# Optimization experiments

Measured on AMD Instinct MI355X. Metric: run time of the kernel, lower is better.

The kernel has to match this reference:

```python
import jax, jax.numpy as jnp
import numpy as np

D_MODEL = 1024
NHEAD = 16
EPS = 1e-5


def pos_embed(x, pos):
    # Faithful, vectorized form of the sparse rotation matrix in the source.
    # Source builds rot[..., i, i+1] = sin(pos*i*omega) for even i and
    # rot[..., i, i-1] = cos(pos*i*omega) for odd i, then contracts the feature
    # dim of x against the rotation (intended einsum 'btf,btfd->btd').
    # Resulting column j: even j <- x[..., j+1]*cos(pos*(j+1)*omega),
    #                     odd  j <- x[..., j-1]*sin(pos*(j-1)*omega).
    d = x.shape[-1]
    omega = jnp.pi / d
    i_even = jnp.arange(0, d, 2, dtype=x.dtype)   # even rows -> odd output cols (sin)
    i_odd = jnp.arange(1, d, 2, dtype=x.dtype)    # odd rows  -> even output cols (cos)
    p = pos[..., None]  # (L,B,1)
    sin_part = jnp.sin(p * i_even * omega) * x[..., 0::2]  # -> odd columns
    cos_part = jnp.cos(p * i_odd * omega) * x[..., 1::2]   # -> even columns
    # interleave: even col = cos_part, odd col = sin_part
    return jnp.stack([cos_part, sin_part], axis=-1).reshape(x.shape)


def layer_norm_eps(x, w, b):
    # Source uses torch.var default (unbiased, ddof=1)
    mean = jnp.mean(x, axis=-1, keepdims=True)
    var = jnp.var(x, axis=-1, keepdims=True, ddof=1)
    return w * (x - mean) / jnp.sqrt(var + EPS) + b


def mha(q, k, v, w_qkv, b_qkv, w_o, b_o, nhead):
    L, B, E = q.shape
    S = k.shape[0]
    hd = E // nhead
    wq, wk, wv = jnp.split(w_qkv, 3, axis=0)
    bq, bk, bv = jnp.split(b_qkv, 3, axis=0)
    qp = (q @ wq.T + bq).reshape(L, B, nhead, hd).transpose(1, 2, 0, 3)  # (B,h,L,hd)
    kp = (k @ wk.T + bk).reshape(S, B, nhead, hd).transpose(1, 2, 0, 3)
    vp = (v @ wv.T + bv).reshape(S, B, nhead, hd).transpose(1, 2, 0, 3)
    scale = jnp.asarray(1.0 / np.sqrt(hd), q.dtype)
    scores = jnp.einsum('bhld,bhsd->bhls', qp, kp) * scale
    attn = jax.nn.softmax(scores, axis=-1)
    out = jnp.einsum('bhls,bhsd->bhld', attn, vp)
    out = out.transpose(2, 0, 1, 3).reshape(L, B, E) @ w_o.T + b_o
    ws = attn.mean(axis=1)  # average over heads, torch default
    return out, ws


def setup_inputs() -> dict:
    key = jax.random.key(0)
    ks = jax.random.split(key, 16)
    T, S, B, E, FF = 1024, 1024, 4, D_MODEL, 4096
    sd = 0.02
    return {
        'tgt': jax.random.normal(ks[0], (T, B, E), jnp.float32),
        'memory': jax.random.normal(ks[1], (S, B, E), jnp.float32),
        'pos': jax.random.uniform(ks[2], (S, B), jnp.float32) * S,
        'query_pos': jax.random.uniform(ks[3], (T, B), jnp.float32) * T,
        'w_qkv_self': jax.random.normal(ks[4], (3 * E, E), jnp.float32) * sd,
        'b_qkv_self': jnp.zeros((3 * E,), jnp.float32),
        'w_o_self': jax.random.normal(ks[5], (E, E), jnp.float32) * sd,
        'b_o_self': jnp.zeros((E,), jnp.float32),
        'w_qkv_cross': jax.random.normal(ks[6], (3 * E, E), jnp.float32) * sd,
        'b_qkv_cross': jnp.zeros((3 * E,), jnp.float32),
        'w_o_cross': jax.random.normal(ks[7], (E, E), jnp.float32) * sd,
        'b_o_cross': jnp.zeros((E,), jnp.float32),
        'w1': jax.random.normal(ks[8], (FF, E), jnp.float32) * sd,
        'b1': jnp.zeros((FF,), jnp.float32),
        'w2': jax.random.normal(ks[9], (E, FF), jnp.float32) * sd,
        'b2': jnp.zeros((E,), jnp.float32),
        'g1': jnp.ones((E,), jnp.float32),
        'beta1': jnp.zeros((E,), jnp.float32),
        'g2': jnp.ones((E,), jnp.float32),
        'beta2': jnp.zeros((E,), jnp.float32),
    }


def reference(tgt, memory, pos, query_pos,
              w_qkv_self, b_qkv_self, w_o_self, b_o_self,
              w_qkv_cross, b_qkv_cross, w_o_cross, b_o_cross,
              w1, b1, w2, b2, g1, beta1, g2, beta2):
    # normalize_before=False, residual=True, dropout inactive (eval)
    qk = pos_embed(tgt, query_pos)
    tgt2, _ = mha(qk, qk, tgt, w_qkv_self, b_qkv_self, w_o_self, b_o_self, NHEAD)
    tgt = tgt + tgt2
    tgt = layer_norm_eps(tgt, g1, beta1)
    tgt2, ws = mha(pos_embed(tgt, query_pos), pos_embed(memory, pos), memory,
                   w_qkv_cross, b_qkv_cross, w_o_cross, b_o_cross, NHEAD)
    tgt = tgt + tgt2
    tgt = layer_norm_eps(tgt, g2, beta2)
    tgt2 = jax.nn.relu(tgt @ w1.T + b1) @ w2.T + b2
    tgt = tgt + tgt2
    return tgt, ws
```

## Files before the change

### kernel.cpp

```cpp
#include <hip/hip_runtime.h>

typedef unsigned short u16;
typedef __attribute__((ext_vector_type(8))) short short8;
typedef __attribute__((ext_vector_type(8))) unsigned short u16x8;
typedef __attribute__((ext_vector_type(4))) float f32x4;

#define GLOAD16(SRC, DST) __builtin_amdgcn_global_load_lds( \
    (const __attribute__((address_space(1))) void*)(SRC),   \
    (__attribute__((address_space(3))) void*)(DST), 16, 0, 0)

#define SWZ(BKv, r) ((BKv) == 32 ? (((r) >> 1) & 3) : ((r) & 7))

#define QSCALE 0.18033688011112042f

__device__ __forceinline__ u16 f2bf(float f) {
  union { float f; unsigned u; } v; v.f = f;
  unsigned r = v.u + 0x7fffu + ((v.u >> 16) & 1u);
  return (u16)(r >> 16);
}
__device__ __forceinline__ float bf2f(u16 h) {
  union { unsigned u; float f; } v; v.u = ((unsigned)h) << 16;
  return v.f;
}

__global__ __launch_bounds__(256) void wcvt_kernel(const float* __restrict__ s0,
                                                   const float* __restrict__ s1,
                                                   const float* __restrict__ s2,
                                                   const float* __restrict__ s3,
                                                   const float* __restrict__ s4,
                                                   const float* __restrict__ s5,
                                                   u16* __restrict__ dst) {
  long i = ((long)blockIdx.x * 256 + threadIdx.x) * 4;
  const float* src; long off;
  if (i < 3145728)        { src = s0; off = 0; }
  else if (i < 4194304)   { src = s1; off = 3145728; }
  else if (i < 7340032)   { src = s2; off = 4194304; }
  else if (i < 8388608)   { src = s3; off = 7340032; }
  else if (i < 12582912)  { src = s4; off = 8388608; }
  else                    { src = s5; off = 12582912; }
  float4 v = *(const float4*)(src + (i - off));
  ushort4 o; o.x = f2bf(v.x); o.y = f2bf(v.y); o.z = f2bf(v.z); o.w = f2bf(v.w);
  *(ushort4*)(dst + i) = o;
}

__global__ __launch_bounds__(256) void pos_embed_kernel(const float* __restrict__ x,
                                                        const float* __restrict__ pos,
                                                        u16* __restrict__ out,
                                                        u16* __restrict__ out2,
                                                        u16* __restrict__ raw) {
  int m = blockIdx.x;
  int tid = threadIdx.x;
  float p = pos[m];
  long base = ((long)m << 10);
  int j = tid * 4;
  float4 xv = *(const float4*)(x + base + j);
  const float inv = 1.0f / 2048.0f;
  float r0 = p * (float)(j + 0) * inv;
  float r1 = p * (float)(j + 1) * inv;
  float r2 = p * (float)(j + 2) * inv;
  float r3 = p * (float)(j + 3) * inv;
  float s1 = __builtin_amdgcn_sinf(r0 - floorf(r0));
  float c0 = __builtin_amdgcn_cosf(r1 - floorf(r1));
  float s3 = __builtin_amdgcn_sinf(r2 - floorf(r2));
  float c2 = __builtin_amdgcn_cosf(r3 - floorf(r3));
  ushort4 o;
  o.x = f2bf(c0 * xv.y);
  o.y = f2bf(s1 * xv.x);
  o.z = f2bf(c2 * xv.w);
  o.w = f2bf(s3 * xv.z);
  *(ushort4*)(out + base + j) = o;
  if (out2) *(ushort4*)(out2 + base + j) = o;
  if (raw) {
    ushort4 rw; rw.x = f2bf(xv.x); rw.y = f2bf(xv.y); rw.z = f2bf(xv.z); rw.w = f2bf(xv.w);
    *(ushort4*)(raw + base + j) = rw;
  }
}

__global__ __launch_bounds__(256) void fattn_kernel(const u16* __restrict__ Q,
                                                    const u16* __restrict__ K,
                                                    const u16* __restrict__ Vt,
                                                    u16* __restrict__ AO,
                                                    float2* __restrict__ Ml) {
  __shared__ u16 lK[2][4096];
  __shared__ u16 lV[2][4096];
  __shared__ u16 lP[4][1024];
  const int tid = threadIdx.x, lane = tid & 63, wid = tid >> 6;
  const int nb = gridDim.x * gridDim.y;
  const int orig = blockIdx.y * gridDim.x + blockIdx.x;
  const int swz = (orig & 7) * (nb >> 3) + (orig >> 3);
  const int qt = swz & 15;
  const int bh = swz >> 4;
  const int b = bh >> 4, h = bh & 15;
  const u16* Qp = Q + ((long)bh << 16);
  const u16* Kp = K + ((long)bh << 16);
  const u16* Vp = Vt + ((long)bh << 16);
  const int q0 = qt << 6;
  const int cr = lane >> 4;

  short8 af0, af1;
  {
    const u16* qs = Qp + (long)(q0 + wid * 16 + (lane & 15)) * 64 + cr * 8;
    af0 = *(const short8*)qs;
    af1 = *(const short8*)(qs + 32);
  }

  float m = -1e30f, l = 0.f;
  f32x4 acco[4] = {};

  auto stage = [&](int bufi, int kv) {
    int s0 = kv << 6;
#pragma unroll
    for (int it = 0; it < 2; it++) {
      int c = it * 256 + tid;
      int row = c >> 3, ch = c & 7;
      int sch = (ch ^ (row & 7)) * 8;
      GLOAD16(Kp + (long)(s0 + row) * 64 + sch, &lK[bufi][c * 8]);
      GLOAD16(Vp + (long)row * 1024 + s0 + sch, &lV[bufi][c * 8]);
    }
  };

  stage(0, 0);
  __syncthreads();
  int buf = 0;
  for (int kv = 0; kv < 16; kv++) {
    if (kv < 15) stage(buf ^ 1, kv + 1);
    f32x4 accs[4];
    __builtin_amdgcn_s_setprio(1);
#pragma unroll
    for (int j = 0; j < 4; j++) {
      int sr = j * 16 + (lane & 15);
      const short8 kf0 = *(const short8*)&lK[buf][sr * 64 + ((cr ^ (sr & 7)) * 8)];
      const short8 kf1 = *(const short8*)&lK[buf][sr * 64 + (((4 + cr) ^ (sr & 7)) * 8)];
      f32x4 zz = {};
      zz = __builtin_amdgcn_mfma_f32_16x16x32_bf16(kf0, af0, zz, 0, 0, 0);
      accs[j] = __builtin_amdgcn_mfma_f32_16x16x32_bf16(kf1, af1, zz, 0, 0, 0);
    }
    __builtin_amdgcn_s_setprio(0);
    float tm = fmaxf(fmaxf(fmaxf(accs[0][0], accs[0][1]), fmaxf(accs[0][2], accs[0][3])),
                     fmaxf(fmaxf(accs[1][0], accs[1][1]), fmaxf(accs[1][2], accs[1][3])));
    float tm2 = fmaxf(fmaxf(fmaxf(accs[2][0], accs[2][1]), fmaxf(accs[2][2], accs[2][3])),
                      fmaxf(fmaxf(accs[3][0], accs[3][1]), fmaxf(accs[3][2], accs[3][3])));
    tm = fmaxf(tm, tm2);
    tm = fmaxf(tm, __shfl_xor(tm, 16));
    tm = fmaxf(tm, __shfl_xor(tm, 32));
    if (!__all(tm - m <= 8.0f)) {
      float mn = fmaxf(m, tm);
      float f = __builtin_amdgcn_exp2f(m - mn);
      m = mn; l *= f;
#pragma unroll
      for (int r = 0; r < 4; r++) {
        float fr = __shfl(f, cr * 4 + r);
        acco[0][r] *= fr; acco[1][r] *= fr; acco[2][r] *= fr; acco[3][r] *= fr;
      }
    }
    float rs = 0.f;
#pragma unroll
    for (int j = 0; j < 4; j++)
#pragma unroll
      for (int r = 0; r < 4; r++) {
        float p = __builtin_amdgcn_exp2f(accs[j][r] - m);
        accs[j][r] = p;
        rs += p;
      }
    rs += __shfl_xor(rs, 16);
    rs += __shfl_xor(rs, 32);
    l += rs;
    {
      u16* pw = lP[wid];
      int q = lane & 15;
      int rowoff = q * 64;
      int qs7 = q & 7;
#pragma unroll
      for (int j = 0; j < 4; j++) {
        uint2 pk;
        asm("v_cvt_pk_bf16_f32 %0, %1, %2"
            : "=v"(pk.x) : "v"(accs[j][0]), "v"(accs[j][1]));
        asm("v_cvt_pk_bf16_f32 %0, %1, %2"
            : "=v"(pk.y) : "v"(accs[j][2]), "v"(accs[j][3]));
        int chunk = 2 * j + (cr >> 1);
        int idx = rowoff + ((chunk ^ qs7) * 8) + 4 * (cr & 1);
        *(uint2*)(pw + idx) = pk;
      }
    }
    {
      int ql = lane & 15;
      const u16* pr = &lP[wid][ql * 64];
      short8 pa0 = *(const short8*)&pr[(cr ^ (ql & 7)) * 8];
      short8 pa1 = *(const short8*)&pr[((4 + cr) ^ (ql & 7)) * 8];
      __builtin_amdgcn_s_setprio(1);
#pragma unroll
      for (int j = 0; j < 4; j++) {
        int dr = j * 16 + (lane & 15);
        const short8 vf0 = *(const short8*)&lV[buf][dr * 64 + ((cr ^ (dr & 7)) * 8)];
        const short8 vf1 = *(const short8*)&lV[buf][dr * 64 + (((4 + cr) ^ (dr & 7)) * 8)];
        acco[j] = __builtin_amdgcn_mfma_f32_16x16x32_bf16(pa0, vf0, acco[j], 0, 0, 0);
        acco[j] = __builtin_amdgcn_mfma_f32_16x16x32_bf16(pa1, vf1, acco[j], 0, 0, 0);
      }
      __builtin_amdgcn_s_setprio(0);
    }
    __syncthreads();
    buf ^= 1;
  }
  float invl = 1.0f / l;
  float ilr[4];
#pragma unroll
  for (int r = 0; r < 4; r++) ilr[r] = __shfl(invl, cr * 4 + r);
#pragma unroll
  for (int j = 0; j < 4; j++)
#pragma unroll
    for (int r = 0; r < 4; r++) {
      int t = q0 + wid * 16 + cr * 4 + r;
      int e = (b << 10) + (h << 6) + j * 16 + (lane & 15);
      AO[(long)t * 4096 + e] = f2bf(acco[j][r] * ilr[r]);
    }
  if (Ml && lane < 16) {
    int t = q0 + wid * 16 + lane;
    Ml[((long)bh << 10) + t] = make_float2(m, invl);
  }
}

__global__ __launch_bounds__(256) void wsrec_kernel(const u16* __restrict__ Q,
                                                    const u16* __restrict__ K,
                                                    const float2* __restrict__ Ml,
                                                    float* __restrict__ ws) {
  __shared__ u16 lK[2][4096];
  const int tid = threadIdx.x, lane = tid & 63, wid = tid >> 6;
  const int nb = gridDim.x * gridDim.y;
  const int orig = blockIdx.y * gridDim.x + blockIdx.x;
  const int swz = (orig & 7) * (nb >> 3) + (orig >> 3);
  const int st = swz & 15, lt = swz >> 4;
  const int b = blockIdx.z;
  const int s0 = st << 6, l0 = lt << 6;
  const int cr = lane >> 4;

  auto stage = [&](int bufi, int h) {
    const u16* Kp = K + (((long)(b * 16 + h)) << 16);
#pragma unroll
    for (int it = 0; it < 2; it++) {
      int c = it * 256 + tid;
      int row = c >> 3, ch = c & 7;
      GLOAD16(Kp + (long)(s0 + row) * 64 + ((ch ^ (row & 7)) * 8), &lK[bufi][c * 8]);
    }
  };

  f32x4 wacc[4] = {};
  stage(0, 0);
  __syncthreads();
  int buf = 0;
  for (int h = 0; h < 16; h++) {
    if (h < 15) stage(buf ^ 1, h + 1);
    const int bh = b * 16 + h;
    short8 af0, af1;
    {
      const u16* qs = Q + ((long)bh << 16) + (long)(l0 + wid * 16 + (lane & 15)) * 64 + cr * 8;
      af0 = *(const short8*)qs;
      af1 = *(const short8*)(qs + 32);
    }
    f32x4 accs[4];
    __builtin_amdgcn_s_setprio(1);
#pragma unroll
    for (int j = 0; j < 4; j++) {
      int sr = j * 16 + (lane & 15);
      const short8 kf0 = *(const short8*)&lK[buf][sr * 64 + ((cr ^ (sr & 7)) * 8)];
      const short8 kf1 = *(const short8*)&lK[buf][sr * 64 + (((4 + cr) ^ (sr & 7)) * 8)];
      f32x4 zz = {};
      zz = __builtin_amdgcn_mfma_f32_16x16x32_bf16(af0, kf0, zz, 0, 0, 0);
      accs[j] = __builtin_amdgcn_mfma_f32_16x16x32_bf16(af1, kf1, zz, 0, 0, 0);
    }
    __builtin_amdgcn_s_setprio(0);
    float mm[4], il[4];
#pragma unroll
    for (int r = 0; r < 4; r++) {
      float2 v = Ml[((long)bh << 10) + l0 + wid * 16 + (lane >> 4) * 4 + r];
      mm[r] = v.x; il[r] = v.y * 0.0625f;
    }
#pragma unroll
    for (int j = 0; j < 4; j++)
#pragma unroll
      for (int r = 0; r < 4; r++)
        wacc[j][r] += __builtin_amdgcn_exp2f(accs[j][r] - mm[r]) * il[r];
    __syncthreads();
    buf ^= 1;
  }
#pragma unroll
  for (int j = 0; j < 4; j++)
#pragma unroll
    for (int r = 0; r < 4; r++) {
      int li = l0 + wid * 16 + (lane >> 4) * 4 + r;
      int si = s0 + j * 16 + (lane & 15);
      ws[((long)b << 20) + (long)li * 1024 + si] = wacc[j][r];
    }
}

__global__ __launch_bounds__(256) void ln_kernel(const float* __restrict__ X,
                                                 const float* __restrict__ D1,
                                                 const float* __restrict__ D2,
                                                 const float* __restrict__ bo,
                                                 const float* __restrict__ g,
                                                 const float* __restrict__ be,
                                                 float* __restrict__ out,
                                                 u16* __restrict__ bfout,
                                                 const float* __restrict__ pepos) {
  int mrow = blockIdx.x;
  int tid = threadIdx.x, lane = tid & 63, wid = tid >> 6;
  long base = ((long)mrow << 10);
  float4 a = *(const float4*)(X + base + tid * 4);
  float4 b = *(const float4*)(D1 + base + tid * 4);
  float x0 = a.x + b.x, x1 = a.y + b.y, x2 = a.z + b.z, x3 = a.w + b.w;
  if (D2) {
    float4 c = *(const float4*)(D2 + base + tid * 4);
    x0 += c.x; x1 += c.y; x2 += c.z; x3 += c.w;
  }
  if (bo) {
    float4 c = *(const float4*)(bo + tid * 4);
    x0 += c.x; x1 += c.y; x2 += c.z; x3 += c.w;
  }
  float s = x0 + x1 + x2 + x3;
#pragma unroll
  for (int o = 32; o; o >>= 1) s += __shfl_xor(s, o);
  __shared__ float red[4];
  if (lane == 0) red[wid] = s;
  __syncthreads();
  float mean = (red[0] + red[1] + red[2] + red[3]) * (1.0f / 1024.0f);
  float d0 = x0 - mean, d1 = x1 - mean, d2 = x2 - mean, d3 = x3 - mean;
  float ss = d0 * d0 + d1 * d1 + d2 * d2 + d3 * d3;
#pragma unroll
  for (int o = 32; o; o >>= 1) ss += __shfl_xor(ss, o);
  __syncthreads();
  if (lane == 0) red[wid] = ss;
  __syncthreads();
  float var = (red[0] + red[1] + red[2] + red[3]) * (1.0f / 1023.0f);
  float sc = 1.0f / sqrtf(var + 1e-5f);
  float4 gv = *(const float4*)(g + tid * 4);
  float4 bv = *(const float4*)(be + tid * 4);
  float y0 = gv.x * d0 * sc + bv.x;
  float y1 = gv.y * d1 * sc + bv.y;
  float y2 = gv.z * d2 * sc + bv.z;
  float y3 = gv.w * d3 * sc + bv.w;
  float4 o4; o4.x = y0; o4.y = y1; o4.z = y2; o4.w = y3;
  *(float4*)(out + base + tid * 4) = o4;
  if (bfout) {
    ushort4 hh;
    if (pepos) {
      float p = pepos[mrow];
      int j = tid * 4;
      const float inv = 1.0f / 2048.0f;
      float r0 = p * (float)(j + 0) * inv;
      float r1 = p * (float)(j + 1) * inv;
      float r2 = p * (float)(j + 2) * inv;
      float r3 = p * (float)(j + 3) * inv;
      float s1 = __builtin_amdgcn_sinf(r0 - floorf(r0));
      float c0 = __builtin_amdgcn_cosf(r1 - floorf(r1));
      float s3 = __builtin_amdgcn_sinf(r2 - floorf(r2));
      float c2 = __builtin_amdgcn_cosf(r3 - floorf(r3));
      hh.x = f2bf(c0 * y1);
      hh.y = f2bf(s1 * y0);
      hh.z = f2bf(c2 * y3);
      hh.w = f2bf(s3 * y2);
    } else {
      hh.x = f2bf(y0); hh.y = f2bf(y1); hh.z = f2bf(y2); hh.w = f2bf(y3);
    }
    *(ushort4*)(bfout + base + tid * 4) = hh;
  }
}

__global__ __launch_bounds__(256) void add3_kernel(const float* __restrict__ X,
                                                   const float* __restrict__ P0,
                                                   const float* __restrict__ P1,
                                                   const float* __restrict__ b,
                                                   float* __restrict__ out) {
  long i = ((long)blockIdx.x * 256 + threadIdx.x) * 4;
  int col = (int)(i & 1023);
  float4 x = *(const float4*)(X + i);
  float4 p = *(const float4*)(P0 + i);
  float4 q = *(const float4*)(P1 + i);
  float4 bb = *(const float4*)(b + col);
  float4 o;
  o.x = x.x + p.x + q.x + bb.x;
  o.y = x.y + p.y + q.y + bb.y;
  o.z = x.z + p.z + q.z + bb.z;
  o.w = x.w + p.w + q.w + bb.w;
  *(float4*)(out + i) = o;
}

template <int BM, int BN, int BK, int WR, int WC, int NT, int DB>
__global__ __launch_bounds__(NT)
void gemm_bt_kernel(const u16* __restrict__ A, const u16* __restrict__ B,
                    void* __restrict__ C, const float* __restrict__ bias,
                    int lda, int ldb, int ldc, int K,
                    long sAz, long sBz, long sCz, long sbz,
                    float alpha, int flags) {
  constexpr int WTM = BM / WR, WTN = BN / WC;
  constexpr int FM = WTM / 16, FN = WTN / 16;
  constexpr int NC = BK / 8;
  __shared__ u16 lA[DB][BM * BK];
  __shared__ u16 lB[DB][BN * BK];
  const int tid = threadIdx.x, lane = tid & 63, wid = tid >> 6;
  const int wr = wid / WC, wc = wid % WC;
  const int z = blockIdx.z;

  const int nwg = gridDim.x * gridDim.y;
  const int orig = blockIdx.y * gridDim.x + blockIdx.x;
  const int qq = nwg >> 3, rr = nwg & 7;
  const int xcd = orig & 7, idx = orig >> 3;
  const int swz = (xcd < rr ? xcd * (qq + 1) : rr * (qq + 1) + (xcd - rr) * qq) + idx;
  const int bxs = swz % gridDim.x;
  const int bys = swz / gridDim.x;

  const u16* Ab = A + z * sAz + (long)bys * BM * lda;
  const u16* Bb = B + z * sBz + (long)bxs * BN * ldb;

  f32x4 acc[FM][FN] = {};

  auto stage = [&](int bufi, int k0) {
#pragma unroll
    for (int c0 = 0; c0 < BM * NC; c0 += NT) {
      int c = c0 + tid;
      if ((BM * NC) % NT == 0 || c < BM * NC) {
        int row = c / NC, ch = c % NC;
        int sch = ch ^ SWZ(BK, row);
        GLOAD16(Ab + (long)row * lda + k0 + sch * 8, &lA[bufi][c * 8]);
      }
    }
#pragma unroll
    for (int c0 = 0; c0 < BN * NC; c0 += NT) {
      int c = c0 + tid;
      if ((BN * NC) % NT == 0 || c < BN * NC) {
        int row = c / NC, ch = c % NC;
        int sch = ch ^ SWZ(BK, row);
        GLOAD16(Bb + (long)row * ldb + k0 + sch * 8, &lB[bufi][c * 8]);
      }
    }
  };

  auto compute = [&](int bufi) {
#pragma unroll
    for (int kk = 0; kk < BK / 32; kk++) {
      short8 afv[FM], bfv[FN];
#pragma unroll
      for (int i = 0; i < FM; i++) {
        int row = wr * WTM + i * 16 + (lane & 15);
        int ch = kk * 4 + (lane >> 4);
        afv[i] = *(const short8*)&lA[bufi][row * BK + ((ch ^ SWZ(BK, row)) * 8)];
      }
#pragma unroll
      for (int j = 0; j < FN; j++) {
        int row = wc * WTN + j * 16 + (lane & 15);
        int ch = kk * 4 + (lane >> 4);
        bfv[j] = *(const short8*)&lB[bufi][row * BK + ((ch ^ SWZ(BK, row)) * 8)];
      }
#pragma unroll
      for (int i = 0; i < FM; i++)
#pragma unroll
        for (int j = 0; j < FN; j++)
          acc[i][j] = __builtin_amdgcn_mfma_f32_16x16x32_bf16(afv[i], bfv[j], acc[i][j], 0, 0, 0);
    }
  };

  const int nk = K / BK;
  if constexpr (DB == 2) {
    stage(0, 0);
    __syncthreads();
    int cur = 0;
    for (int t = 0; t < nk; t++) {
      if (t + 1 < nk) stage(cur ^ 1, (t + 1) * BK);
      compute(cur);
      __syncthreads();
      cur ^= 1;
    }
  } else {
    for (int t = 0; t < nk; t++) {
      stage(0, t * BK);
      __syncthreads();
      compute(0);
      __syncthreads();
    }
  }

  const long rbase = (long)bys * BM + wr * WTM;
  const int cbase = bxs * BN + wc * WTN;
  const float* bz = bias ? (bias + z * sbz) : nullptr;
#pragma unroll
  for (int i = 0; i < FM; i++)
#pragma unroll
    for (int j = 0; j < FN; j++)
#pragma unroll
      for (int r = 0; r < 4; r++) {
        long row = rbase + i * 16 + ((lane >> 4) * 4 + r);
        int col = cbase + j * 16 + (lane & 15);
        float v = acc[i][j][r];
        if (!(flags & 8)) v *= alpha;
        if (flags & 1) v += bz[col];
        if ((flags & 8) && z == 0) v *= alpha;
        if (flags & 2) v = fmaxf(v, 0.0f);
        if (flags & 16) {
          int t = (int)(row >> 2), bb = (int)(row & 3);
          int hh = col >> 6, dd = col & 63;
          long base16 = ((long)(bb * 16 + hh)) << 16;
          long off = (long)z * 4194304 + base16 +
                     (z == 2 ? (long)dd * 1024 + t : (long)t * 64 + dd);
          ((u16*)C)[off] = f2bf(v);
        } else {
          long off = (long)z * sCz + row * (long)ldc + col;
          if (flags & 4) ((float*)C)[off] = v;
          else ((u16*)C)[off] = f2bf(v);
        }
      }
}

extern "C" void kernel_launch(void* const* d_in, const int* in_sizes, int n_in,
                              void* d_out, int out_size, void* d_ws, size_t ws_size,
                              hipStream_t stream) {
  const float* tgt  = (const float*)d_in[0];
  const float* mem  = (const float*)d_in[1];
  const float* pos  = (const float*)d_in[2];
  const float* qpos = (const float*)d_in[3];
  const float* wqkvS = (const float*)d_in[4];
  const float* bqkvS = (const float*)d_in[5];
  const float* woS   = (const float*)d_in[6];
  const float* boS   = (const float*)d_in[7];
  const float* wqkvC = (const float*)d_in[8];
  const float* bqkvC = (const float*)d_in[9];
  const float* woC   = (const float*)d_in[10];
  const float* boC   = (const float*)d_in[11];
  const float* w1  = (const float*)d_in[12];
  const float* b1  = (const float*)d_in[13];
  const float* w2  = (const float*)d_in[14];
  const float* b2  = (const float*)d_in[15];
  const float* g1  = (const float*)d_in[16];
  const float* be1 = (const float*)d_in[17];
  const float* g2  = (const float*)d_in[18];
  const float* be2 = (const float*)d_in[19];

  const size_t MB = 1024ull * 1024ull;
  float* out0 = (float*)d_out;
  float* wsout = out0 + 4194304;

  char* W = (char*)d_ws;
  u16* wb = (u16*)W;
  u16* wqkvS_b = wb;
  u16* woS_b   = wb + 3145728;
  u16* wqkvC_b = wb + 4194304;
  u16* woC_b   = wb + 7340032;
  u16* w1_b    = wb + 8388608;
  u16* w2_b    = wb + 12582912;
  float* Xf   = (float*)(W + 32 * MB);
  float* OPar = (float*)(W + 48 * MB);
  u16* bf1 = (u16*)(W + 80 * MB);
  u16* bf2 = (u16*)(W + 88 * MB);
  u16* bf3 = (u16*)(W + 96 * MB);
  float2* Ml = (float2*)(W + 96 * MB);
  u16* Qb  = (u16*)(W + 104 * MB);
  u16* Kb  = (u16*)(W + 112 * MB);
  u16* Vtb = (u16*)(W + 120 * MB);
  u16* AOb = (u16*)(W + 128 * MB);
  u16* F1  = (u16*)(W + 104 * MB);

  wcvt_kernel<<<16384, 256, 0, stream>>>(wqkvS, woS, wqkvC, woC, w1, w2, wb);

  pos_embed_kernel<<<4096, 256, 0, stream>>>(tgt, qpos, bf1, bf2, bf3);
  gemm_bt_kernel<128, 128, 32, 2, 4, 512, 2><<<dim3(8, 32, 3), 512, 0, stream>>>(
      bf1, wqkvS_b, Qb, bqkvS, 1024, 1024, 0, 1024,
      4194304, 1048576, 0, 1024, QSCALE, 1 | 8 | 16);
  fattn_kernel<<<dim3(16, 64), 256, 0, stream>>>(Qb, Kb, Vtb, AOb, nullptr);
  gemm_bt_kernel<128, 128, 32, 2, 4, 512, 2><<<dim3(8, 32, 2), 512, 0, stream>>>(
      AOb, woS_b, OPar, nullptr, 1024, 1024, 1024, 512,
      512, 512, 4194304, 0, 1.0f, 4);
  ln_kernel<<<4096, 256, 0, stream>>>(tgt, OPar, OPar + 4194304, boS, g1, be1,
                                      Xf, bf1, qpos);

  pos_embed_kernel<<<4096, 256, 0, stream>>>(mem, pos, bf2, nullptr, bf3);
  gemm_bt_kernel<128, 128, 32, 2, 4, 512, 2><<<dim3(8, 32, 3), 512, 0, stream>>>(
      bf1, wqkvC_b, Qb, bqkvC, 1024, 1024, 0, 1024,
      4194304, 1048576, 0, 1024, QSCALE, 1 | 8 | 16);
  fattn_kernel<<<dim3(16, 64), 256, 0, stream>>>(Qb, Kb, Vtb, AOb, Ml);
  wsrec_kernel<<<dim3(16, 16, 4), 256, 0, stream>>>(Qb, Kb, Ml, wsout);
  gemm_bt_kernel<128, 128, 32, 2, 4, 512, 2><<<dim3(8, 32, 2), 512, 0, stream>>>(
      AOb, woC_b, OPar, nullptr, 1024, 1024, 1024, 512,
      512, 512, 4194304, 0, 1.0f, 4);
  ln_kernel<<<4096, 256, 0, stream>>>(Xf, OPar, OPar + 4194304, boC, g2, be2,
                                      Xf, bf1, nullptr);

  gemm_bt_kernel<128, 128, 32, 2, 4, 512, 2><<<dim3(32, 32, 1), 512, 0, stream>>>(
      bf1, w1_b, F1, b1, 1024, 1024, 4096, 1024, 0, 0, 0, 0, 1.0f, 1 | 2);
  gemm_bt_kernel<128, 128, 32, 2, 4, 512, 2><<<dim3(8, 32, 2), 512, 0, stream>>>(
      F1, w2_b, OPar, nullptr, 4096, 4096, 1024, 2048,
      2048, 2048, 4194304, 0, 1.0f, 4);
  add3_kernel<<<4096, 256, 0, stream>>>(Xf, OPar, OPar + 4194304, b2, out0);
}
```

Baseline: 403.2 us.

## Add 256x256 GEMM kernel with interleaved staging and MFMA for QKV and FFN1

Adds a dedicated 256x256x64 bf16 GEMM kernel for the QKV projections and the first FFN layer. Global-to-LDS loads for the next K-tile are split into four chunks and interleaved between quadrant MFMA groups, using manual vmcnt waits, raw barriers and priority hints. Larger tiles raise arithmetic intensity and cut per-tile sync overhead, at the cost of many more accumulator registers, fewer workgroups (192 or 256 blocks), and possible register spills. The generic kernel is kept for the remaining GEMMs with its single-buffer path and scatter epilogue removed.

After: 467.9 us. 16.1% more time.

```diff
diff --git a/kernel.cpp b/kernel.cpp
--- a/kernel.cpp
+++ b/kernel.cpp
@@ -383,107 +383,115 @@
   *(float4*)(out + i) = o;
 }
 
-template <int BM, int BN, int BK, int WR, int WC, int NT, int DB>
-__global__ __launch_bounds__(NT)
-void gemm_bt_kernel(const u16* __restrict__ A, const u16* __restrict__ B,
-                    void* __restrict__ C, const float* __restrict__ bias,
-                    int lda, int ldb, int ldc, int K,
-                    long sAz, long sBz, long sCz, long sbz,
-                    float alpha, int flags) {
-  constexpr int WTM = BM / WR, WTN = BN / WC;
-  constexpr int FM = WTM / 16, FN = WTN / 16;
-  constexpr int NC = BK / 8;
-  __shared__ u16 lA[DB][BM * BK];
-  __shared__ u16 lB[DB][BN * BK];
+__global__ __launch_bounds__(512, 2)
+void gemm8_kernel(const u16* __restrict__ A, const u16* __restrict__ B,
+                  void* __restrict__ C, const float* __restrict__ bias,
+                  int lda, int ldb, int ldc, int K,
+                  long sAz, long sBz, long sCz, long sbz,
+                  float alpha, int flags) {
+  __shared__ u16 lA[2][16384];
+  __shared__ u16 lB[2][16384];
   const int tid = threadIdx.x, lane = tid & 63, wid = tid >> 6;
-  const int wr = wid / WC, wc = wid % WC;
+  const int wr = wid >> 2, wc = wid & 3;
   const int z = blockIdx.z;
-
   const int nwg = gridDim.x * gridDim.y;
   const int orig = blockIdx.y * gridDim.x + blockIdx.x;
-  const int qq = nwg >> 3, rr = nwg & 7;
-  const int xcd = orig & 7, idx = orig >> 3;
-  const int swz = (xcd < rr ? xcd * (qq + 1) : rr * (qq + 1) + (xcd - rr) * qq) + idx;
+  const int sq = nwg >> 3, sr = nwg & 7;
+  const int xcd = orig & 7, sidx = orig >> 3;
+  const int swz = (xcd < sr ? xcd * (sq + 1) : sr * (sq + 1) + (xcd - sr) * sq) + sidx;
   const int bxs = swz % gridDim.x;
   const int bys = swz / gridDim.x;
-
-  const u16* Ab = A + z * sAz + (long)bys * BM * lda;
-  const u16* Bb = B + z * sBz + (long)bxs * BN * ldb;
-
-  f32x4 acc[FM][FN] = {};
-
-  auto stage = [&](int bufi, int k0) {
-#pragma unroll
-    for (int c0 = 0; c0 < BM * NC; c0 += NT) {
-      int c = c0 + tid;
-      if ((BM * NC) % NT == 0 || c < BM * NC) {
-        int row = c / NC, ch = c % NC;
-        int sch = ch ^ SWZ(BK, row);
-        GLOAD16(Ab + (long)row * lda + k0 + sch * 8, &lA[bufi][c * 8]);
-      }
-    }
-#pragma unroll
-    for (int c0 = 0; c0 < BN * NC; c0 += NT) {
-      int c = c0 + tid;
-      if ((BN * NC) % NT == 0 || c < BN * NC) {
-        int row = c / NC, ch = c % NC;
-        int sch = ch ^ SWZ(BK, row);
-        GLOAD16(Bb + (long)row * ldb + k0 + sch * 8, &lB[bufi][c * 8]);
+  const u16* Ab = A + z * sAz + (long)bys * 256 * lda;
+  const u16* Bb = B + z * sBz + (long)bxs * 256 * ldb;
+
+  f32x4 acc[8][4] = {};
+
+  auto stage2 = [&](int bufi, int k0, int r0) {
+#pragma unroll
+    for (int q = 0; q < 2; q++) {
+      int c = (r0 + q) * 512 + tid;
+      if (c < 2048) {
+        int row = c >> 3, ch = c & 7;
+        GLOAD16(Ab + (long)row * lda + k0 + ((ch ^ (row & 7)) * 8), &lA[bufi][c * 8]);
+      } else {
+        int c2 = c - 2048;
+        int row = c2 >> 3, ch = c2 & 7;
+        GLOAD16(Bb + (long)row * ldb + k0 + ((ch ^ (row & 7)) * 8), &lB[bufi][c2 * 8]);
       }
     }
   };
-
-  auto compute = [&](int bufi) {
-#pragma unroll
-    for (int kk = 0; kk < BK / 32; kk++) {
-      short8 afv[FM], bfv[FN];
-#pragma unroll
-      for (int i = 0; i < FM; i++) {
-        int row = wr * WTM + i * 16 + (lane & 15);
-        int ch = kk * 4 + (lane >> 4);
-        afv[i] = *(const short8*)&lA[bufi][row * BK + ((ch ^ SWZ(BK, row)) * 8)];
-      }
-#pragma unroll
-      for (int j = 0; j < FN; j++) {
-        int row = wc * WTN + j * 16 + (lane & 15);
-        int ch = kk * 4 + (lane >> 4);
-        bfv[j] = *(const short8*)&lB[bufi][row * BK + ((ch ^ SWZ(BK, row)) * 8)];
-      }
-#pragma unroll
-      for (int i = 0; i < FM; i++)
-#pragma unroll
-        for (int j = 0; j < FN; j++)
-          acc[i][j] = __builtin_amdgcn_mfma_f32_16x16x32_bf16(afv[i], bfv[j], acc[i][j], 0, 0, 0);
-    }
+  auto loadA = [&](int bufi, int qa, short8* af) {
+#pragma unroll
+    for (int f = 0; f < 4; f++)
+#pragma unroll
+      for (int g = 0; g < 2; g++) {
+        int row = wr * 128 + qa * 64 + f * 16 + (lane & 15);
+        int ch = (g * 4 + (lane >> 4)) ^ (row & 7);
+        af[f * 2 + g] = *(const short8*)&lA[bufi][row * 64 + ch * 8];
+      }
   };
-
-  const int nk = K / BK;
-  if constexpr (DB == 2) {
-    stage(0, 0);
-    __syncthreads();
-    int cur = 0;
-    for (int t = 0; t < nk; t++) {
-      if (t + 1 < nk) stage(cur ^ 1, (t + 1) * BK);
-      compute(cur);
-      __syncthreads();
-      cur ^= 1;
-    }
-  } else {
-    for (int t = 0; t < nk; t++) {
-      stage(0, t * BK);
-      __syncthreads();
-      compute(0);
-      __syncthreads();
-    }
-  }
-
-  const long rbase = (long)bys * BM + wr * WTM;
-  const int cbase = bxs * BN + wc * WTN;
+  auto loadB = [&](int bufi, int qb, short8* bf) {
+#pragma unroll
+    for (int f = 0; f < 2; f++)
+#pragma unroll
+      for (int g = 0; g < 2; g++) {
+        int row = wc * 64 + qb * 32 + f * 16 + (lane & 15);
+        int ch = (g * 4 + (lane >> 4)) ^ (row & 7);
+        bf[f * 2 + g] = *(const short8*)&lB[bufi][row * 64 + ch * 8];
+      }
+  };
+  auto mfma16 = [&](int qa, int qb, short8* af, short8* bf) {
+    __builtin_amdgcn_s_setprio(1);
+#pragma unroll
+    for (int f = 0; f < 4; f++)
+#pragma unroll
+      for (int e = 0; e < 2; e++)
+#pragma unroll
+        for (int g = 0; g < 2; g++)
+          acc[qa * 4 + f][qb * 2 + e] = __builtin_amdgcn_mfma_f32_16x16x32_bf16(
+              af[f * 2 + g], bf[e * 2 + g], acc[qa * 4 + f][qb * 2 + e], 0, 0, 0);
+    __builtin_amdgcn_s_setprio(0);
+  };
+
+  const int nk = K / 64;
+#pragma unroll
+  for (int r = 0; r < 8; r += 2) stage2(0, 0, r);
+  for (int t = 0; t < nk; t++) {
+    const int buf = t & 1;
+    const bool more = (t + 1 < nk);
+    const int k1 = (t + 1) * 64;
+    short8 af[8], bf[4];
+    if (more) {
+      stage2(buf ^ 1, k1, 0);
+      asm volatile("s_waitcnt vmcnt(2)" ::: "memory");
+    } else {
+      asm volatile("s_waitcnt vmcnt(0)" ::: "memory");
+    }
+    __builtin_amdgcn_s_barrier();
+    __builtin_amdgcn_sched_barrier(0);
+    loadA(buf, 0, af);
+    loadB(buf, 0, bf);
+    mfma16(0, 0, af, bf);
+    if (more) stage2(buf ^ 1, k1, 2);
+    loadB(buf, 1, bf);
+    mfma16(0, 1, af, bf);
+    if (more) stage2(buf ^ 1, k1, 4);
+    loadA(buf, 1, af);
+    mfma16(1, 1, af, bf);
+    if (more) stage2(buf ^ 1, k1, 6);
+    loadB(buf, 0, bf);
+    mfma16(1, 0, af, bf);
+    __builtin_amdgcn_sched_barrier(0);
+    __builtin_amdgcn_s_barrier();
+  }
+
+  const long rbase = (long)bys * 256 + wr * 128;
+  const int cbase = bxs * 256 + wc * 64;
   const float* bz = bias ? (bias + z * sbz) : nullptr;
 #pragma unroll
-  for (int i = 0; i < FM; i++)
-#pragma unroll
-    for (int j = 0; j < FN; j++)
+  for (int i = 0; i < 8; i++)
+#pragma unroll
+    for (int j = 0; j < 4; j++)
 #pragma unroll
       for (int r = 0; r < 4; r++) {
         long row = rbase + i * 16 + ((lane >> 4) * 4 + r);
@@ -505,6 +513,113 @@
           if (flags & 4) ((float*)C)[off] = v;
           else ((u16*)C)[off] = f2bf(v);
         }
+      }
+}
+
+template <int BM, int BN, int BK, int WR, int WC, int NT, int DB>
+__global__ __launch_bounds__(NT)
+void gemm_bt_kernel(const u16* __restrict__ A, const u16* __restrict__ B,
+                    void* __restrict__ C, const float* __restrict__ bias,
+                    int lda, int ldb, int ldc, int K,
+                    long sAz, long sBz, long sCz, long sbz,
+                    float alpha, int flags) {
+  constexpr int WTM = BM / WR, WTN = BN / WC;
+  constexpr int FM = WTM / 16, FN = WTN / 16;
+  constexpr int NC = BK / 8;
+  __shared__ u16 lA[DB][BM * BK];
+  __shared__ u16 lB[DB][BN * BK];
+  const int tid = threadIdx.x, lane = tid & 63, wid = tid >> 6;
+  const int wr = wid / WC, wc = wid % WC;
+  const int z = blockIdx.z;
+
+  const int nwg = gridDim.x * gridDim.y;
+  const int orig = blockIdx.y * gridDim.x + blockIdx.x;
+  const int qq = nwg >> 3, rr = nwg & 7;
+  const int xcd = orig & 7, idx = orig >> 3;
+  const int swz = (xcd < rr ? xcd * (qq + 1) : rr * (qq + 1) + (xcd - rr) * qq) + idx;
+  const int bxs = swz % gridDim.x;
+  const int bys = swz / gridDim.x;
+
+  const u16* Ab = A + z * sAz + (long)bys * BM * lda;
+  const u16* Bb = B + z * sBz + (long)bxs * BN * ldb;
+
+  f32x4 acc[FM][FN] = {};
+
+  auto stage = [&](int bufi, int k0) {
+#pragma unroll
+    for (int c0 = 0; c0 < BM * NC; c0 += NT) {
+      int c = c0 + tid;
+      if ((BM * NC) % NT == 0 || c < BM * NC) {
+        int row = c / NC, ch = c % NC;
+        int sch = ch ^ SWZ(BK, row);
+        GLOAD16(Ab + (long)row * lda + k0 + sch * 8, &lA[bufi][c * 8]);
+      }
+    }
+#pragma unroll
+    for (int c0 = 0; c0 < BN * NC; c0 += NT) {
+      int c = c0 + tid;
+      if ((BN * NC) % NT == 0 || c < BN * NC) {
+        int row = c / NC, ch = c % NC;
+        int sch = ch ^ SWZ(BK, row);
+        GLOAD16(Bb + (long)row * ldb + k0 + sch * 8, &lB[bufi][c * 8]);
+      }
+    }
+  };
+
+  auto compute = [&](int bufi) {
+#pragma unroll
+    for (int kk = 0; kk < BK / 32; kk++) {
+      short8 afv[FM], bfv[FN];
+#pragma unroll
+      for (int i = 0; i < FM; i++) {
+        int row = wr * WTM + i * 16 + (lane & 15);
+        int ch = kk * 4 + (lane >> 4);
+        afv[i] = *(const short8*)&lA[bufi][row * BK + ((ch ^ SWZ(BK, row)) * 8)];
+      }
+#pragma unroll
+      for (int j = 0; j < FN; j++) {
+        int row = wc * WTN + j * 16 + (lane & 15);
+        int ch = kk * 4 + (lane >> 4);
+        bfv[j] = *(const short8*)&lB[bufi][row * BK + ((ch ^ SWZ(BK, row)) * 8)];
+      }
+#pragma unroll
+      for (int i = 0; i < FM; i++)
+#pragma unroll
+        for (int j = 0; j < FN; j++)
+          acc[i][j] = __builtin_amdgcn_mfma_f32_16x16x32_bf16(afv[i], bfv[j], acc[i][j], 0, 0, 0);
+    }
+  };
+
+  const int nk = K / BK;
+  stage(0, 0);
+  __syncthreads();
+  int cur = 0;
+  for (int t = 0; t < nk; t++) {
+    if (t + 1 < nk) stage(cur ^ 1, (t + 1) * BK);
+    compute(cur);
+    __syncthreads();
+    cur ^= 1;
+  }
+
+  const long rbase = (long)bys * BM + wr * WTM;
+  const int cbase = bxs * BN + wc * WTN;
+  const float* bz = bias ? (bias + z * sbz) : nullptr;
+#pragma unroll
+  for (int i = 0; i < FM; i++)
+#pragma unroll
+    for (int j = 0; j < FN; j++)
+#pragma unroll
+      for (int r = 0; r < 4; r++) {
+        long row = rbase + i * 16 + ((lane >> 4) * 4 + r);
+        int col = cbase + j * 16 + (lane & 15);
+        float v = acc[i][j][r];
+        if (!(flags & 8)) v *= alpha;
+        if (flags & 1) v += bz[col];
+        if ((flags & 8) && z == 0) v *= alpha;
+        if (flags & 2) v = fmaxf(v, 0.0f);
+        long off = (long)z * sCz + row * (long)ldc + col;
+        if (flags & 4) ((float*)C)[off] = v;
+        else ((u16*)C)[off] = f2bf(v);
       }
 }
 
@@ -559,7 +674,7 @@
   wcvt_kernel<<<16384, 256, 0, stream>>>(wqkvS, woS, wqkvC, woC, w1, w2, wb);
 
   pos_embed_kernel<<<4096, 256, 0, stream>>>(tgt, qpos, bf1, bf2, bf3);
-  gemm_bt_kernel<128, 128, 32, 2, 4, 512, 2><<<dim3(8, 32, 3), 512, 0, stream>>>(
+  gemm8_kernel<<<dim3(4, 16, 3), 512, 0, stream>>>(
       bf1, wqkvS_b, Qb, bqkvS, 1024, 1024, 0, 1024,
       4194304, 1048576, 0, 1024, QSCALE, 1 | 8 | 16);
   fattn_kernel<<<dim3(16, 64), 256, 0, stream>>>(Qb, Kb, Vtb, AOb, nullptr);
@@ -570,7 +685,7 @@
                                       Xf, bf1, qpos);
 
   pos_embed_kernel<<<4096, 256, 0, stream>>>(mem, pos, bf2, nullptr, bf3);
-  gemm_bt_kernel<128, 128, 32, 2, 4, 512, 2><<<dim3(8, 32, 3), 512, 0, stream>>>(
+  gemm8_kernel<<<dim3(4, 16, 3), 512, 0, stream>>>(
       bf1, wqkvC_b, Qb, bqkvC, 1024, 1024, 0, 1024,
       4194304, 1048576, 0, 1024, QSCALE, 1 | 8 | 16);
   fattn_kernel<<<dim3(16, 64), 256, 0, stream>>>(Qb, Kb, Vtb, AOb, Ml);
@@ -581,7 +696,7 @@
   ln_kernel<<<4096, 256, 0, stream>>>(Xf, OPar, OPar + 4194304, boC, g2, be2,
                                       Xf, bf1, nullptr);
 
-  gemm_bt_kernel<128, 128, 32, 2, 4, 512, 2><<<dim3(32, 32, 1), 512, 0, stream>>>(
+  gemm8_kernel<<<dim3(16, 16, 1), 512, 0, stream>>>(
       bf1, w1_b, F1, b1, 1024, 1024, 4096, 1024, 0, 0, 0, 0, 1.0f, 1 | 2);
   gemm_bt_kernel<128, 128, 32, 2, 4, 512, 2><<<dim3(8, 32, 2), 512, 0, stream>>>(
       F1, w2_b, OPar, nullptr, 4096, 4096, 1024, 2048,
```

## Process two query tiles per wave in flash attention to reuse K/V tiles

Applied to the files above, without the earlier changes.

Each fattn block now handles 128 query rows instead of 64. Every wave keeps two independent 16-row query fragments, each with its own online-softmax state, and both share the K and V tiles staged in LDS, so K/V global loads and LDS reads are amortised over twice as many MFMAs. The grid is halved, the P scratch buffer is doubled, and register pressure rises, which may reduce occupancy and leaves fewer blocks to fill the CUs. The GEMM kernel also drops its non-double-buffered branch, which is a cleanup because DB is always 2 at the call sites.

New measurement: 404.9 us. No clear change (+0.4%).

```diff
diff --git a/kernel.cpp b/kernel.cpp
--- a/kernel.cpp
+++ b/kernel.cpp
@@ -83,29 +83,31 @@
                                                     float2* __restrict__ Ml) {
   __shared__ u16 lK[2][4096];
   __shared__ u16 lV[2][4096];
-  __shared__ u16 lP[4][1024];
+  __shared__ u16 lP[8][1024];
   const int tid = threadIdx.x, lane = tid & 63, wid = tid >> 6;
   const int nb = gridDim.x * gridDim.y;
   const int orig = blockIdx.y * gridDim.x + blockIdx.x;
   const int swz = (orig & 7) * (nb >> 3) + (orig >> 3);
-  const int qt = swz & 15;
-  const int bh = swz >> 4;
+  const int qt = swz & 7;
+  const int bh = swz >> 3;
   const int b = bh >> 4, h = bh & 15;
   const u16* Qp = Q + ((long)bh << 16);
   const u16* Kp = K + ((long)bh << 16);
   const u16* Vp = Vt + ((long)bh << 16);
-  const int q0 = qt << 6;
+  const int q0 = qt << 7;
   const int cr = lane >> 4;
 
-  short8 af0, af1;
+  short8 aAf0, aAf1, aBf0, aBf1;
   {
     const u16* qs = Qp + (long)(q0 + wid * 16 + (lane & 15)) * 64 + cr * 8;
-    af0 = *(const short8*)qs;
-    af1 = *(const short8*)(qs + 32);
-  }
-
-  float m = -1e30f, l = 0.f;
-  f32x4 acco[4] = {};
+    aAf0 = *(const short8*)qs;
+    aAf1 = *(const short8*)(qs + 32);
+    aBf0 = *(const short8*)(qs + 4096);
+    aBf1 = *(const short8*)(qs + 4096 + 32);
+  }
+
+  float mA = -1e30f, lA_ = 0.f, mB = -1e30f, lB_ = 0.f;
+  f32x4 accA[4] = {}, accB[4] = {};
 
   auto stage = [&](int bufi, int kv) {
     int s0 = kv << 6;
@@ -124,98 +126,150 @@
   int buf = 0;
   for (int kv = 0; kv < 16; kv++) {
     if (kv < 15) stage(buf ^ 1, kv + 1);
-    f32x4 accs[4];
+    f32x4 sA[4], sB[4];
     __builtin_amdgcn_s_setprio(1);
 #pragma unroll
     for (int j = 0; j < 4; j++) {
       int sr = j * 16 + (lane & 15);
       const short8 kf0 = *(const short8*)&lK[buf][sr * 64 + ((cr ^ (sr & 7)) * 8)];
       const short8 kf1 = *(const short8*)&lK[buf][sr * 64 + (((4 + cr) ^ (sr & 7)) * 8)];
-      f32x4 zz = {};
-      zz = __builtin_amdgcn_mfma_f32_16x16x32_bf16(kf0, af0, zz, 0, 0, 0);
-      accs[j] = __builtin_amdgcn_mfma_f32_16x16x32_bf16(kf1, af1, zz, 0, 0, 0);
+      f32x4 zA = {}, zB = {};
+      zA = __builtin_amdgcn_mfma_f32_16x16x32_bf16(kf0, aAf0, zA, 0, 0, 0);
+      zB = __builtin_amdgcn_mfma_f32_16x16x32_bf16(kf0, aBf0, zB, 0, 0, 0);
+      sA[j] = __builtin_amdgcn_mfma_f32_16x16x32_bf16(kf1, aAf1, zA, 0, 0, 0);
+      sB[j] = __builtin_amdgcn_mfma_f32_16x16x32_bf16(kf1, aBf1, zB, 0, 0, 0);
     }
     __builtin_amdgcn_s_setprio(0);
-    float tm = fmaxf(fmaxf(fmaxf(accs[0][0], accs[0][1]), fmaxf(accs[0][2], accs[0][3])),
-                     fmaxf(fmaxf(accs[1][0], accs[1][1]), fmaxf(accs[1][2], accs[1][3])));
-    float tm2 = fmaxf(fmaxf(fmaxf(accs[2][0], accs[2][1]), fmaxf(accs[2][2], accs[2][3])),
-                      fmaxf(fmaxf(accs[3][0], accs[3][1]), fmaxf(accs[3][2], accs[3][3])));
-    tm = fmaxf(tm, tm2);
-    tm = fmaxf(tm, __shfl_xor(tm, 16));
-    tm = fmaxf(tm, __shfl_xor(tm, 32));
-    if (!__all(tm - m <= 8.0f)) {
-      float mn = fmaxf(m, tm);
-      float f = __builtin_amdgcn_exp2f(m - mn);
-      m = mn; l *= f;
-#pragma unroll
-      for (int r = 0; r < 4; r++) {
-        float fr = __shfl(f, cr * 4 + r);
-        acco[0][r] *= fr; acco[1][r] *= fr; acco[2][r] *= fr; acco[3][r] *= fr;
-      }
-    }
-    float rs = 0.f;
-#pragma unroll
-    for (int j = 0; j < 4; j++)
-#pragma unroll
-      for (int r = 0; r < 4; r++) {
-        float p = __builtin_amdgcn_exp2f(accs[j][r] - m);
-        accs[j][r] = p;
-        rs += p;
-      }
-    rs += __shfl_xor(rs, 16);
-    rs += __shfl_xor(rs, 32);
-    l += rs;
     {
-      u16* pw = lP[wid];
+      float tm = fmaxf(fmaxf(fmaxf(sA[0][0], sA[0][1]), fmaxf(sA[0][2], sA[0][3])),
+                       fmaxf(fmaxf(sA[1][0], sA[1][1]), fmaxf(sA[1][2], sA[1][3])));
+      float t2 = fmaxf(fmaxf(fmaxf(sA[2][0], sA[2][1]), fmaxf(sA[2][2], sA[2][3])),
+                       fmaxf(fmaxf(sA[3][0], sA[3][1]), fmaxf(sA[3][2], sA[3][3])));
+      tm = fmaxf(tm, t2);
+      tm = fmaxf(tm, __shfl_xor(tm, 16));
+      tm = fmaxf(tm, __shfl_xor(tm, 32));
+      if (!__all(tm - mA <= 8.0f)) {
+        float mn = fmaxf(mA, tm);
+        float f = __builtin_amdgcn_exp2f(mA - mn);
+        mA = mn; lA_ *= f;
+#pragma unroll
+        for (int r = 0; r < 4; r++) {
+          float fr = __shfl(f, cr * 4 + r);
+          accA[0][r] *= fr; accA[1][r] *= fr; accA[2][r] *= fr; accA[3][r] *= fr;
+        }
+      }
+      float rs = 0.f;
+#pragma unroll
+      for (int j = 0; j < 4; j++)
+#pragma unroll
+        for (int r = 0; r < 4; r++) {
+          float p = __builtin_amdgcn_exp2f(sA[j][r] - mA);
+          sA[j][r] = p;
+          rs += p;
+        }
+      rs += __shfl_xor(rs, 16);
+      rs += __shfl_xor(rs, 32);
+      lA_ += rs;
+    }
+    {
+      float tm = fmaxf(fmaxf(fmaxf(sB[0][0], sB[0][1]), fmaxf(sB[0][2], sB[0][3])),
+                       fmaxf(fmaxf(sB[1][0], sB[1][1]), fmaxf(sB[1][2], sB[1][3])));
+      float t2 = fmaxf(fmaxf(fmaxf(sB[2][0], sB[2][1]), fmaxf(sB[2][2], sB[2][3])),
+                       fmaxf(fmaxf(sB[3][0], sB[3][1]), fmaxf(sB[3][2], sB[3][3])));
+      tm = fmaxf(tm, t2);
+      tm = fmaxf(tm, __shfl_xor(tm, 16));
+      tm = fmaxf(tm, __shfl_xor(tm, 32));
+      if (!__all(tm - mB <= 8.0f)) {
+        float mn = fmaxf(mB, tm);
+        float f = __builtin_amdgcn_exp2f(mB - mn);
+        mB = mn; lB_ *= f;
+#pragma unroll
+        for (int r = 0; r < 4; r++) {
+          float fr = __shfl(f, cr * 4 + r);
+          accB[0][r] *= fr; accB[1][r] *= fr; accB[2][r] *= fr; accB[3][r] *= fr;
+        }
+      }
+      float rs = 0.f;
+#pragma unroll
+      for (int j = 0; j < 4; j++)
+#pragma unroll
+        for (int r = 0; r < 4; r++) {
+          float p = __builtin_amdgcn_exp2f(sB[j][r] - mB);
+          sB[j][r] = p;
+          rs += p;
+        }
+      rs += __shfl_xor(rs, 16);
+      rs += __shfl_xor(rs, 32);
+      lB_ += rs;
+    }
+    {
       int q = lane & 15;
       int rowoff = q * 64;
       int qs7 = q & 7;
+      u16* pwA = lP[wid];
+      u16* pwB = lP[4 + wid];
 #pragma unroll
       for (int j = 0; j < 4; j++) {
-        uint2 pk;
-        asm("v_cvt_pk_bf16_f32 %0, %1, %2"
-            : "=v"(pk.x) : "v"(accs[j][0]), "v"(accs[j][1]));
-        asm("v_cvt_pk_bf16_f32 %0, %1, %2"
-            : "=v"(pk.y) : "v"(accs[j][2]), "v"(accs[j][3]));
         int chunk = 2 * j + (cr >> 1);
         int idx = rowoff + ((chunk ^ qs7) * 8) + 4 * (cr & 1);
-        *(uint2*)(pw + idx) = pk;
+        uint2 pkA, pkB;
+        asm("v_cvt_pk_bf16_f32 %0, %1, %2"
+            : "=v"(pkA.x) : "v"(sA[j][0]), "v"(sA[j][1]));
+        asm("v_cvt_pk_bf16_f32 %0, %1, %2"
+            : "=v"(pkA.y) : "v"(sA[j][2]), "v"(sA[j][3]));
+        asm("v_cvt_pk_bf16_f32 %0, %1, %2"
+            : "=v"(pkB.x) : "v"(sB[j][0]), "v"(sB[j][1]));
+        asm("v_cvt_pk_bf16_f32 %0, %1, %2"
+            : "=v"(pkB.y) : "v"(sB[j][2]), "v"(sB[j][3]));
+        *(uint2*)(pwA + idx) = pkA;
+        *(uint2*)(pwB + idx) = pkB;
       }
     }
     {
       int ql = lane & 15;
-      const u16* pr = &lP[wid][ql * 64];
-      short8 pa0 = *(const short8*)&pr[(cr ^ (ql & 7)) * 8];
-      short8 pa1 = *(const short8*)&pr[((4 + cr) ^ (ql & 7)) * 8];
+      const u16* prA = &lP[wid][ql * 64];
+      const u16* prB = &lP[4 + wid][ql * 64];
+      short8 paA0 = *(const short8*)&prA[(cr ^ (ql & 7)) * 8];
+      short8 paA1 = *(const short8*)&prA[((4 + cr) ^ (ql & 7)) * 8];
+      short8 paB0 = *(const short8*)&prB[(cr ^ (ql & 7)) * 8];
+      short8 paB1 = *(const short8*)&prB[((4 + cr) ^ (ql & 7)) * 8];
       __builtin_amdgcn_s_setprio(1);
 #pragma unroll
       for (int j = 0; j < 4; j++) {
         int dr = j * 16 + (lane & 15);
         const short8 vf0 = *(const short8*)&lV[buf][dr * 64 + ((cr ^ (dr & 7)) * 8)];
         const short8 vf1 = *(const short8*)&lV[buf][dr * 64 + (((4 + cr) ^ (dr & 7)) * 8)];
-        acco[j] = __builtin_amdgcn_mfma_f32_16x16x32_bf16(pa0, vf0, acco[j], 0, 0, 0);
-        acco[j] = __builtin_amdgcn_mfma_f32_16x16x32_bf16(pa1, vf1, acco[j], 0, 0, 0);
+        accA[j] = __builtin_amdgcn_mfma_f32_16x16x32_bf16(paA0, vf0, accA[j], 0, 0, 0);
+        accB[j] = __builtin_amdgcn_mfma_f32_16x16x32_bf16(paB0, vf0, accB[j], 0, 0, 0);
+        accA[j] = __builtin_amdgcn_mfma_f32_16x16x32_bf16(paA1, vf1, accA[j], 0, 0, 0);
+        accB[j] = __builtin_amdgcn_mfma_f32_16x16x32_bf16(paB1, vf1, accB[j], 0, 0, 0);
       }
       __builtin_amdgcn_s_setprio(0);
     }
     __syncthreads();
     buf ^= 1;
   }
-  float invl = 1.0f / l;
-  float ilr[4];
-#pragma unroll
-  for (int r = 0; r < 4; r++) ilr[r] = __shfl(invl, cr * 4 + r);
+  float invA = 1.0f / lA_, invB = 1.0f / lB_;
+  float iA[4], iB[4];
+#pragma unroll
+  for (int r = 0; r < 4; r++) {
+    iA[r] = __shfl(invA, cr * 4 + r);
+    iB[r] = __shfl(invB, cr * 4 + r);
+  }
+  const int ecol = (b << 10) + (h << 6);
 #pragma unroll
   for (int j = 0; j < 4; j++)
 #pragma unroll
     for (int r = 0; r < 4; r++) {
       int t = q0 + wid * 16 + cr * 4 + r;
-      int e = (b << 10) + (h << 6) + j * 16 + (lane & 15);
-      AO[(long)t * 4096 + e] = f2bf(acco[j][r] * ilr[r]);
+      int e = ecol + j * 16 + (lane & 15);
+      AO[(long)t * 4096 + e] = f2bf(accA[j][r] * iA[r]);
+      AO[(long)(t + 64) * 4096 + e] = f2bf(accB[j][r] * iB[r]);
     }
   if (Ml && lane < 16) {
     int t = q0 + wid * 16 + lane;
-    Ml[((long)bh << 10) + t] = make_float2(m, invl);
+    Ml[((long)bh << 10) + t] = make_float2(mA, invA);
+    Ml[((long)bh << 10) + t + 64] = make_float2(mB, invB);
   }
 }
 
@@ -458,23 +512,14 @@
   };
 
   const int nk = K / BK;
-  if constexpr (DB == 2) {
-    stage(0, 0);
+  stage(0, 0);
+  __syncthreads();
+  int cur = 0;
+  for (int t = 0; t < nk; t++) {
+    if (t + 1 < nk) stage(cur ^ 1, (t + 1) * BK);
+    compute(cur);
     __syncthreads();
-    int cur = 0;
-    for (int t = 0; t < nk; t++) {
-      if (t + 1 < nk) stage(cur ^ 1, (t + 1) * BK);
-      compute(cur);
-      __syncthreads();
-      cur ^= 1;
-    }
-  } else {
-    for (int t = 0; t < nk; t++) {
-      stage(0, t * BK);
-      __syncthreads();
-      compute(0);
-      __syncthreads();
-    }
+    cur ^= 1;
   }
 
   const long rbase = (long)bys * BM + wr * WTM;
@@ -562,7 +607,7 @@
   gemm_bt_kernel<128, 128, 32, 2, 4, 512, 2><<<dim3(8, 32, 3), 512, 0, stream>>>(
       bf1, wqkvS_b, Qb, bqkvS, 1024, 1024, 0, 1024,
       4194304, 1048576, 0, 1024, QSCALE, 1 | 8 | 16);
-  fattn_kernel<<<dim3(16, 64), 256, 0, stream>>>(Qb, Kb, Vtb, AOb, nullptr);
+  fattn_kernel<<<dim3(8, 64), 256, 0, stream>>>(Qb, Kb, Vtb, AOb, nullptr);
   gemm_bt_kernel<128, 128, 32, 2, 4, 512, 2><<<dim3(8, 32, 2), 512, 0, stream>>>(
       AOb, woS_b, OPar, nullptr, 1024, 1024, 1024, 512,
       512, 512, 4194304, 0, 1.0f, 4);
@@ -573,7 +618,7 @@
   gemm_bt_kernel<128, 128, 32, 2, 4, 512, 2><<<dim3(8, 32, 3), 512, 0, stream>>>(
       bf1, wqkvC_b, Qb, bqkvC, 1024, 1024, 0, 1024,
       4194304, 1048576, 0, 1024, QSCALE, 1 | 8 | 16);
-  fattn_kernel<<<dim3(16, 64), 256, 0, stream>>>(Qb, Kb, Vtb, AOb, Ml);
+  fattn_kernel<<<dim3(8, 64), 256, 0, stream>>>(Qb, Kb, Vtb, AOb, Ml);
   wsrec_kernel<<<dim3(16, 16, 4), 256, 0, stream>>>(Qb, Kb, Ml, wsout);
   gemm_bt_kernel<128, 128, 32, 2, 4, 512, 2><<<dim3(8, 32, 2), 512, 0, stream>>>(
       AOb, woC_b, OPar, nullptr, 1024, 1024, 1024, 512,
```
